# Performance work log

Measured on AMD Instinct MI355X. Metric: run time of the kernel, lower is better.

## Reference

```python
import jax, jax.numpy as jnp
import numpy as np
import math

D_MODEL = 1024
N_HEADS = 16
B, L, K = 2, 512, 4


def sinusoidal_pe(n, dim):
    # matches SinusoidalEmbedding buffer pe[:n]
    position = jnp.arange(n, dtype=jnp.float32)[:, None]
    div_term = jnp.exp(jnp.arange(0, dim, 2, dtype=jnp.float32) * (-math.log(10000.0) / dim))
    ang = position * div_term  # [n, dim//2]
    pe = jnp.zeros((n, dim), dtype=jnp.float32)
    pe = pe.at[:, 0::2].set(jnp.sin(ang))
    pe = pe.at[:, 1::2].set(jnp.cos(ang))
    return pe


def setup_inputs() -> dict:
    key = jax.random.key(0)
    ks = jax.random.split(key, 8)
    s = 1.0 / math.sqrt(D_MODEL)
    return {
        "h": jax.random.normal(ks[0], (B, L, K, D_MODEL), dtype=jnp.float32),
        "probs": jax.random.uniform(ks[1], (B, L, K), dtype=jnp.float32),
        "Wq": jax.random.normal(ks[2], (D_MODEL, D_MODEL), dtype=jnp.float32) * s,
        "bq": jnp.zeros((D_MODEL,), dtype=jnp.float32),
        "Wk": jax.random.normal(ks[3], (D_MODEL, D_MODEL), dtype=jnp.float32) * s,
        "bk": jnp.zeros((D_MODEL,), dtype=jnp.float32),
        "Wv": jax.random.normal(ks[4], (D_MODEL, D_MODEL), dtype=jnp.float32) * s,
        "bv": jnp.zeros((D_MODEL,), dtype=jnp.float32),
        "Wo": jax.random.normal(ks[5], (D_MODEL, D_MODEL), dtype=jnp.float32) * s,
        "bo": jnp.zeros((D_MODEL,), dtype=jnp.float32),
        "prob_bias_scale": jnp.float32(1.0),
        "n_heads": N_HEADS,
    }


def reference(h, probs, Wq, bq, Wk, bk, Wv, bv, Wo, bo, prob_bias_scale, n_heads):
    Bh, Lh, kh, D = h.shape
    N = Lh * kh
    hd = D // n_heads
    scale = hd ** (-0.5)

    h_flat = h.reshape(Bh, N, D) + sinusoidal_pe(N, D)[None]  # [B, N, D]
    probs_flat = probs.reshape(Bh, N)

    # torch Linear: x @ W.T + b
    q = (h_flat @ Wq.T + bq).reshape(Bh, N, n_heads, hd).transpose(0, 2, 1, 3)
    key = (h_flat @ Wk.T + bk).reshape(Bh, N, n_heads, hd).transpose(0, 2, 1, 3)
    v = (h_flat @ Wv.T + bv).reshape(Bh, N, n_heads, hd).transpose(0, 2, 1, 3)

    scores = jnp.einsum("bhnd,bhmd->bhnm", q, key) * scale  # [B,H,N,N]
    prob_bias = jnp.log(probs_flat + 1e-8)[:, None, None, :]  # bias on key axis
    scores = scores + prob_bias_scale * prob_bias
    attn = jax.nn.softmax(scores, axis=-1)  # dropout is identity in eval
    out = jnp.einsum("bhnm,bhmd->bhnd", attn, v)
    out = out.transpose(0, 2, 1, 3).reshape(Bh, N, D)
    out = out @ Wo.T + bo
    return out.reshape(Bh, Lh, kh, D)
```

## Files before the change

kernel.cpp:

```cpp
#include <hip/hip_runtime.h>

typedef _Float16 h8 __attribute__((ext_vector_type(8)));
typedef _Float16 h4 __attribute__((ext_vector_type(4)));
typedef __fp16 fp16x2 __attribute__((ext_vector_type(2)));
typedef float f32x4 __attribute__((ext_vector_type(4)));

#define NSEQ 2048
#define DMODEL 1024
#define HD 64
#define C2 0.1803368801111244f

#define OFF_HPE  (size_t)0
#define OFF_WQ   (size_t)8388608
#define OFF_WK   (size_t)10485760
#define OFF_WV   (size_t)12582912
#define OFF_WO   (size_t)14680064
#define OFF_Q    (size_t)16777216
#define OFF_K    (size_t)25165824
#define OFF_VT   (size_t)33554432
#define OFF_AO   (size_t)41943040
#define OFF_PB   (size_t)50331648

#define GLL(g, l) __builtin_amdgcn_global_load_lds( \
    (const __attribute__((address_space(1))) unsigned int*)(const void*)(g), \
    (__attribute__((address_space(3))) unsigned int*)(l), 16, 0, 0)

__global__ void hpe_kernel(const float* __restrict__ h, _Float16* __restrict__ hpe) {
    int idx = blockIdx.x * blockDim.x + threadIdx.x;
    int row = idx >> 7;
    int c8 = (idx & 127) * 8;
    int n = row & (NSEQ - 1);
    const float kL = -0.025952563241307517f;
    const float kInv2Pi = 0.15915494309189535f;
    union { float4 f4[2]; float f[8]; } in;
    in.f4[0] = *(const float4*)&h[(size_t)row * DMODEL + c8];
    in.f4[1] = *(const float4*)&h[(size_t)row * DMODEL + c8 + 4];
    union { _Float16 hh[8]; uint4 u; } out;
    #pragma unroll
    for (int p = 0; p < 4; ++p) {
        int i2 = (c8 >> 1) + p;
        float div = __builtin_amdgcn_exp2f((float)i2 * kL);
        float rev = (float)n * div * kInv2Pi;
        float rf = __builtin_amdgcn_fractf(rev);
        float s = __builtin_amdgcn_sinf(rf);
        float c = __builtin_amdgcn_cosf(rf);
        out.hh[2 * p]     = (_Float16)(in.f[2 * p] + s);
        out.hh[2 * p + 1] = (_Float16)(in.f[2 * p + 1] + c);
    }
    *(uint4*)&hpe[(size_t)row * DMODEL + c8] = out.u;
}

__global__ void cast4_kernel(const float* __restrict__ w0, const float* __restrict__ w1,
                             const float* __restrict__ w2, const float* __restrict__ w3,
                             _Float16* __restrict__ d0, _Float16* __restrict__ d1,
                             _Float16* __restrict__ d2, _Float16* __restrict__ d3) {
    int i = blockIdx.x * blockDim.x + threadIdx.x;
    int which = i >> 18, idx = i & 262143;
    const float* s = which == 0 ? w0 : which == 1 ? w1 : which == 2 ? w2 : w3;
    _Float16* d    = which == 0 ? d0 : which == 1 ? d1 : which == 2 ? d2 : d3;
    float sc = which == 0 ? C2 : 1.0f;
    float4 v = ((const float4*)s)[idx];
    union { _Float16 hh[4]; uint2 u; } o;
    o.hh[0] = (_Float16)(v.x * sc); o.hh[1] = (_Float16)(v.y * sc);
    o.hh[2] = (_Float16)(v.z * sc); o.hh[3] = (_Float16)(v.w * sc);
    ((uint2*)d)[idx] = o.u;
}

__global__ void pb_kernel(const float* __restrict__ probs, const float* __restrict__ pbs,
                          float* __restrict__ pb) {
    int i = blockIdx.x * blockDim.x + threadIdx.x;
    pb[i] = pbs[0] * log2f(probs[i] + 1e-8f);
}

__global__ __launch_bounds__(256) void gemm_qkv(
    const _Float16* __restrict__ A,
    const _Float16* __restrict__ Wqp, const _Float16* __restrict__ Wkp, const _Float16* __restrict__ Wvp,
    const float* __restrict__ bqp, const float* __restrict__ bkp, const float* __restrict__ bvp,
    _Float16* __restrict__ qb, _Float16* __restrict__ kb, _Float16* __restrict__ vt)
{
    __shared__ __align__(16) _Float16 As[128][64];
    __shared__ __align__(16) _Float16 Bs[128][64];
    int bid = blockIdx.x + 32 * blockIdx.y;
    int nf = (bid & 7) * 96 + (bid >> 3);
    int bx = nf & 31, byy = nf >> 5;
    int widx = byy >> 3;
    const _Float16* W = widx == 0 ? Wqp : widx == 1 ? Wkp : Wvp;
    const float* bias = widx == 0 ? bqp : widx == 1 ? bkp : bvp;
    float bscale = widx == 0 ? C2 : 1.0f;
    int tm = bx * 128;
    int tn = (byy & 7) * 128;
    int t = threadIdx.x;
    int wave = t >> 6, lane = t & 63;
    int wr = (wave >> 1) * 64, wc = (wave & 1) * 64;
    int lr = lane & 15, lg = lane >> 4;

    f32x4 acc[4][4] = {};

    int grow = lane >> 3;
    int gcol = (lane & 7) * 8;
    const _Float16* Aptr = A + (size_t)(tm + wave * 8 + grow) * DMODEL + gcol;
    const _Float16* Wptr = W + (size_t)(tn + wave * 8 + grow) * DMODEL + gcol;

    for (int k0 = 0; k0 < DMODEL; k0 += 64) {
        __syncthreads();
        #pragma unroll
        for (int i = 0; i < 4; ++i)
            GLL(Aptr + (size_t)i * 32 * DMODEL + k0, &As[i * 32 + wave * 8][0]);
        #pragma unroll
        for (int i = 0; i < 4; ++i)
            GLL(Wptr + (size_t)i * 32 * DMODEL + k0, &Bs[i * 32 + wave * 8][0]);
        __syncthreads();
        #pragma unroll
        for (int kk = 0; kk < 2; ++kk) {
            h8 af[4], bf[4];
            #pragma unroll
            for (int mi = 0; mi < 4; ++mi) af[mi] = *(const h8*)&As[wr + mi * 16 + lr][kk * 32 + lg * 8];
            #pragma unroll
            for (int ni = 0; ni < 4; ++ni) bf[ni] = *(const h8*)&Bs[wc + ni * 16 + lr][kk * 32 + lg * 8];
            #pragma unroll
            for (int mi = 0; mi < 4; ++mi)
                #pragma unroll
                for (int ni = 0; ni < 4; ++ni)
                    acc[mi][ni] = __builtin_amdgcn_mfma_f32_16x16x32_f16(af[mi], bf[ni], acc[mi][ni], 0, 0, 0);
        }
    }

    #pragma unroll
    for (int mi = 0; mi < 4; ++mi)
        #pragma unroll
        for (int ni = 0; ni < 4; ++ni) {
            int col = tn + wc + ni * 16 + lr;
            float bv = bias[col] * bscale;
            if (widx < 2) {
                _Float16* dst = widx == 0 ? qb : kb;
                #pragma unroll
                for (int j = 0; j < 4; ++j) {
                    int row = tm + wr + mi * 16 + lg * 4 + j;
                    dst[(size_t)row * DMODEL + col] = (_Float16)(acc[mi][ni][j] + bv);
                }
            } else {
                int row0 = tm + wr + mi * 16 + lg * 4;
                int b = row0 >> 11, n0 = row0 & 2047;
                h4 pk;
                #pragma unroll
                for (int j = 0; j < 4; ++j) pk[j] = (_Float16)(acc[mi][ni][j] + bv);
                *(h4*)&vt[((size_t)b * 1024 + col) * 2048 + n0] = pk;
            }
        }
}

__global__ __launch_bounds__(256) void gemm_ao(
    const _Float16* __restrict__ A, const _Float16* __restrict__ W,
    const float* __restrict__ bias, float* __restrict__ C)
{
    __shared__ __align__(16) _Float16 As[64][64];
    __shared__ __align__(16) _Float16 Bs[128][64];
    int bid = blockIdx.x + 64 * blockIdx.y;
    int nf = (bid & 7) * 64 + (bid >> 3);
    int tm = (nf & 63) * 64;
    int tn = (nf >> 6) * 128;
    int t = threadIdx.x;
    int wave = t >> 6, lane = t & 63;
    int wr = (wave >> 1) * 32, wc = (wave & 1) * 64;
    int lr = lane & 15, lg = lane >> 4;

    f32x4 acc[2][4] = {};

    int grow = lane >> 3;
    int gcol = (lane & 7) * 8;
    const _Float16* Aptr = A + (size_t)(tm + wave * 8 + grow) * DMODEL + gcol;
    const _Float16* Wptr = W + (size_t)(tn + wave * 8 + grow) * DMODEL + gcol;

    for (int k0 = 0; k0 < DMODEL; k0 += 64) {
        __syncthreads();
        #pragma unroll
        for (int i = 0; i < 2; ++i)
            GLL(Aptr + (size_t)i * 32 * DMODEL + k0, &As[i * 32 + wave * 8][0]);
        #pragma unroll
        for (int i = 0; i < 4; ++i)
            GLL(Wptr + (size_t)i * 32 * DMODEL + k0, &Bs[i * 32 + wave * 8][0]);
        __syncthreads();
        #pragma unroll
        for (int kk = 0; kk < 2; ++kk) {
            h8 af[2], bf[4];
            #pragma unroll
            for (int mi = 0; mi < 2; ++mi) af[mi] = *(const h8*)&As[wr + mi * 16 + lr][kk * 32 + lg * 8];
            #pragma unroll
            for (int ni = 0; ni < 4; ++ni) bf[ni] = *(const h8*)&Bs[wc + ni * 16 + lr][kk * 32 + lg * 8];
            #pragma unroll
            for (int mi = 0; mi < 2; ++mi)
                #pragma unroll
                for (int ni = 0; ni < 4; ++ni)
                    acc[mi][ni] = __builtin_amdgcn_mfma_f32_16x16x32_f16(af[mi], bf[ni], acc[mi][ni], 0, 0, 0);
        }
    }

    #pragma unroll
    for (int mi = 0; mi < 2; ++mi)
        #pragma unroll
        for (int ni = 0; ni < 4; ++ni)
            #pragma unroll
            for (int j = 0; j < 4; ++j) {
                int row = tm + wr + mi * 16 + lg * 4 + j;
                int col = tn + wc + ni * 16 + lr;
                C[(size_t)row * DMODEL + col] = acc[mi][ni][j] + bias[col];
            }
}

#define KT 64

#define SWZ(row, bytecol) ((row) * 128 + ((bytecol) ^ (((row) & 7) << 4)))

__global__ __launch_bounds__(512) void flash_kernel(
    const _Float16* __restrict__ Qb,
    const _Float16* __restrict__ Kb,
    const _Float16* __restrict__ Vt,
    const float* __restrict__ pb,
    _Float16* __restrict__ AO)
{
    __shared__ __align__(16) char KsB[2][8192];
    __shared__ __align__(16) char VsB[2][8192];
    __shared__ __align__(16) _Float16 Ps[8][16][72];

    int bid = blockIdx.x + 16 * blockIdx.y;
    int nf = (bid & 7) * 64 + (bid >> 3);
    int qx = nf & 15, bh = nf >> 4;
    int b = bh >> 4, h = bh & 15;
    int q0 = qx * 128;
    int t = threadIdx.x, wave = t >> 6, lane = t & 63;
    int lr = lane & 15, lg = lane >> 4;

    const _Float16* Khead  = Kb + (size_t)b * NSEQ * DMODEL + h * HD;
    const _Float16* Vthead = Vt + ((size_t)b * 1024 + h * HD) * NSEQ;
    const float* pbb = pb + b * NSEQ;

    const _Float16* Qrow = Qb + ((size_t)b * NSEQ + q0 + wave * 16 + lr) * DMODEL + h * HD;
    h8 qf0 = *(const h8*)&Qrow[lg * 8];
    h8 qf1 = *(const h8*)&Qrow[32 + lg * 8];

    const h8 vones = { (_Float16)1, (_Float16)1, (_Float16)1, (_Float16)1,
                       (_Float16)1, (_Float16)1, (_Float16)1, (_Float16)1 };

    float mrun = -INFINITY;
    f32x4 oacc[4] = {};
    f32x4 lsum = {};

    int srow = t >> 3;
    int schunk = (t & 7) ^ (srow & 7);
    const _Float16* Ksrc = Khead + (size_t)srow * DMODEL + schunk * 8;
    const _Float16* Vsrc = Vthead + (size_t)srow * NSEQ + schunk * 8;

    GLL(Ksrc, KsB[0] + wave * 1024);
    GLL(Vsrc, VsB[0] + wave * 1024);
    asm volatile("s_waitcnt vmcnt(0)" ::: "memory");
    __syncthreads();

    int cur = 0;
    for (int kt = 0; kt < 32; ++kt) {
        int k0 = kt * KT;
        if (kt < 31) {
            GLL(Ksrc + (size_t)(k0 + KT) * DMODEL, KsB[cur ^ 1] + wave * 1024);
            GLL(Vsrc + (k0 + KT), VsB[cur ^ 1] + wave * 1024);
        }
        const char* Kc = KsB[cur];
        const char* Vc = VsB[cur];

        f32x4 s[4];
        #pragma unroll
        for (int ci = 0; ci < 4; ++ci)
            s[ci] = *(const f32x4*)&pbb[k0 + ci * 16 + lg * 4];
        #pragma unroll
        for (int ci = 0; ci < 4; ++ci) {
            h8 kf = *(const h8*)(Kc + SWZ(ci * 16 + lr, lg * 16));
            s[ci] = __builtin_amdgcn_mfma_f32_16x16x32_f16(kf, qf0, s[ci], 0, 0, 0);
        }
        #pragma unroll
        for (int ci = 0; ci < 4; ++ci) {
            h8 kf = *(const h8*)(Kc + SWZ(ci * 16 + lr, 64 + lg * 16));
            s[ci] = __builtin_amdgcn_mfma_f32_16x16x32_f16(kf, qf1, s[ci], 0, 0, 0);
        }

        float sm = s[0][0];
        #pragma unroll
        for (int ci = 0; ci < 4; ++ci)
            #pragma unroll
            for (int j = 0; j < 4; ++j) sm = fmaxf(sm, s[ci][j]);
        sm = fmaxf(sm, __shfl_xor(sm, 16));
        sm = fmaxf(sm, __shfl_xor(sm, 32));

        bool need = __any(sm > mrun);
        float newm = need ? fmaxf(mrun, sm) : mrun;

        #pragma unroll
        for (int ci = 0; ci < 4; ++ci) {
            fp16x2 a = __builtin_amdgcn_cvt_pkrtz(__builtin_amdgcn_exp2f(s[ci][0] - newm),
                                                  __builtin_amdgcn_exp2f(s[ci][1] - newm));
            fp16x2 b2 = __builtin_amdgcn_cvt_pkrtz(__builtin_amdgcn_exp2f(s[ci][2] - newm),
                                                   __builtin_amdgcn_exp2f(s[ci][3] - newm));
            union { fp16x2 hh[2]; uint2 u; } pk;
            pk.hh[0] = a; pk.hh[1] = b2;
            *(uint2*)&Ps[wave][lr][ci * 16 + lg * 4] = pk.u;
        }

        h8 vf[2][4];
        #pragma unroll
        for (int kb = 0; kb < 2; ++kb)
            #pragma unroll
            for (int ni = 0; ni < 4; ++ni)
                vf[kb][ni] = *(const h8*)(Vc + SWZ(ni * 16 + lr, kb * 64 + lg * 16));

        if (need) {
            float fs = __builtin_amdgcn_exp2f(mrun - newm);
            mrun = newm;
            #pragma unroll
            for (int j = 0; j < 4; ++j) {
                float fsj = __shfl(fs, (lane & 48) | (lg * 4 + j), 64);
                #pragma unroll
                for (int ni = 0; ni < 4; ++ni) oacc[ni][j] *= fsj;
                lsum[j] *= fsj;
            }
        }

        asm volatile("s_waitcnt lgkmcnt(0)" ::: "memory");
        __builtin_amdgcn_sched_barrier(0);

        #pragma unroll
        for (int kb = 0; kb < 2; ++kb) {
            h8 pa = *(const h8*)&Ps[wave][lr][kb * 32 + lg * 8];
            #pragma unroll
            for (int ni = 0; ni < 4; ++ni)
                oacc[ni] = __builtin_amdgcn_mfma_f32_16x16x32_f16(pa, vf[kb][ni], oacc[ni], 0, 0, 0);
            lsum = __builtin_amdgcn_mfma_f32_16x16x32_f16(pa, vones, lsum, 0, 0, 0);
        }

        asm volatile("s_waitcnt vmcnt(0)" ::: "memory");
        __syncthreads();
        cur ^= 1;
    }

    #pragma unroll
    for (int j = 0; j < 4; ++j) {
        float inv = 1.0f / lsum[j];
        int row = q0 + wave * 16 + lg * 4 + j;
        #pragma unroll
        for (int ni = 0; ni < 4; ++ni)
            AO[((size_t)b * NSEQ + row) * DMODEL + h * HD + ni * 16 + lr] = (_Float16)(oacc[ni][j] * inv);
    }
}

extern "C" void kernel_launch(void* const* d_in, const int* in_sizes, int n_in,
                              void* d_out, int out_size, void* d_ws, size_t ws_size,
                              hipStream_t stream) {
    const float* h    = (const float*)d_in[0];
    const float* prob = (const float*)d_in[1];
    const float* Wq   = (const float*)d_in[2];
    const float* bq   = (const float*)d_in[3];
    const float* Wk   = (const float*)d_in[4];
    const float* bk   = (const float*)d_in[5];
    const float* Wv   = (const float*)d_in[6];
    const float* bv   = (const float*)d_in[7];
    const float* Wo   = (const float*)d_in[8];
    const float* bo   = (const float*)d_in[9];
    const float* pbs  = (const float*)d_in[10];

    char* ws = (char*)d_ws;
    _Float16* hpe  = (_Float16*)(ws + OFF_HPE);
    _Float16* wq16 = (_Float16*)(ws + OFF_WQ);
    _Float16* wk16 = (_Float16*)(ws + OFF_WK);
    _Float16* wv16 = (_Float16*)(ws + OFF_WV);
    _Float16* wo16 = (_Float16*)(ws + OFF_WO);
    _Float16* qb   = (_Float16*)(ws + OFF_Q);
    _Float16* kb16 = (_Float16*)(ws + OFF_K);
    _Float16* vt   = (_Float16*)(ws + OFF_VT);
    _Float16* ao   = (_Float16*)(ws + OFF_AO);
    float*    pbuf = (float*)(ws + OFF_PB);

    hpe_kernel<<<dim3(2048), dim3(256), 0, stream>>>(h, hpe);
    cast4_kernel<<<dim3(4096), dim3(256), 0, stream>>>(Wq, Wk, Wv, Wo, wq16, wk16, wv16, wo16);
    pb_kernel<<<dim3(16), dim3(256), 0, stream>>>(prob, pbs, pbuf);

    gemm_qkv<<<dim3(32, 24), dim3(256), 0, stream>>>(hpe, wq16, wk16, wv16, bq, bk, bv, qb, kb16, vt);

    flash_kernel<<<dim3(16, 32), dim3(512), 0, stream>>>(qb, kb16, vt, pbuf, ao);

    gemm_ao<<<dim3(64, 8), dim3(256), 0, stream>>>(ao, wo16, bo, (float*)d_out);
}
```

Measured before the change: 233.8 us.

## Fuse prep kernels, enlarge QKV GEMM tile, reorder flash loop sync with setprio

```diff
diff --git a/kernel.cpp b/kernel.cpp
--- a/kernel.cpp
+++ b/kernel.cpp
@@ -25,69 +25,69 @@
     (const __attribute__((address_space(1))) unsigned int*)(const void*)(g), \
     (__attribute__((address_space(3))) unsigned int*)(l), 16, 0, 0)
 
-__global__ void hpe_kernel(const float* __restrict__ h, _Float16* __restrict__ hpe) {
+__global__ void prep_kernel(const float* __restrict__ h, _Float16* __restrict__ hpe,
+                            const float* __restrict__ w0, const float* __restrict__ w1,
+                            const float* __restrict__ w2, const float* __restrict__ w3,
+                            _Float16* __restrict__ d0, _Float16* __restrict__ d1,
+                            _Float16* __restrict__ d2, _Float16* __restrict__ d3,
+                            const float* __restrict__ probs, const float* __restrict__ pbs,
+                            float* __restrict__ pb) {
     int idx = blockIdx.x * blockDim.x + threadIdx.x;
-    int row = idx >> 7;
-    int c8 = (idx & 127) * 8;
-    int n = row & (NSEQ - 1);
-    const float kL = -0.025952563241307517f;
-    const float kInv2Pi = 0.15915494309189535f;
-    union { float4 f4[2]; float f[8]; } in;
-    in.f4[0] = *(const float4*)&h[(size_t)row * DMODEL + c8];
-    in.f4[1] = *(const float4*)&h[(size_t)row * DMODEL + c8 + 4];
-    union { _Float16 hh[8]; uint4 u; } out;
-    #pragma unroll
-    for (int p = 0; p < 4; ++p) {
-        int i2 = (c8 >> 1) + p;
-        float div = __builtin_amdgcn_exp2f((float)i2 * kL);
-        float rev = (float)n * div * kInv2Pi;
-        float rf = __builtin_amdgcn_fractf(rev);
-        float s = __builtin_amdgcn_sinf(rf);
-        float c = __builtin_amdgcn_cosf(rf);
-        out.hh[2 * p]     = (_Float16)(in.f[2 * p] + s);
-        out.hh[2 * p + 1] = (_Float16)(in.f[2 * p + 1] + c);
-    }
-    *(uint4*)&hpe[(size_t)row * DMODEL + c8] = out.u;
-}
-
-__global__ void cast4_kernel(const float* __restrict__ w0, const float* __restrict__ w1,
-                             const float* __restrict__ w2, const float* __restrict__ w3,
-                             _Float16* __restrict__ d0, _Float16* __restrict__ d1,
-                             _Float16* __restrict__ d2, _Float16* __restrict__ d3) {
-    int i = blockIdx.x * blockDim.x + threadIdx.x;
-    int which = i >> 18, idx = i & 262143;
-    const float* s = which == 0 ? w0 : which == 1 ? w1 : which == 2 ? w2 : w3;
-    _Float16* d    = which == 0 ? d0 : which == 1 ? d1 : which == 2 ? d2 : d3;
-    float sc = which == 0 ? C2 : 1.0f;
-    float4 v = ((const float4*)s)[idx];
-    union { _Float16 hh[4]; uint2 u; } o;
-    o.hh[0] = (_Float16)(v.x * sc); o.hh[1] = (_Float16)(v.y * sc);
-    o.hh[2] = (_Float16)(v.z * sc); o.hh[3] = (_Float16)(v.w * sc);
-    ((uint2*)d)[idx] = o.u;
-}
-
-__global__ void pb_kernel(const float* __restrict__ probs, const float* __restrict__ pbs,
-                          float* __restrict__ pb) {
-    int i = blockIdx.x * blockDim.x + threadIdx.x;
-    pb[i] = pbs[0] * log2f(probs[i] + 1e-8f);
-}
-
-__global__ __launch_bounds__(256) void gemm_qkv(
+    if (idx < 524288) {
+        int row = idx >> 7;
+        int c8 = (idx & 127) * 8;
+        int n = row & (NSEQ - 1);
+        const float kL = -0.025952563241307517f;
+        const float kInv2Pi = 0.15915494309189535f;
+        union { float4 f4[2]; float f[8]; } in;
+        in.f4[0] = *(const float4*)&h[(size_t)row * DMODEL + c8];
+        in.f4[1] = *(const float4*)&h[(size_t)row * DMODEL + c8 + 4];
+        union { _Float16 hh[8]; uint4 u; } out;
+        #pragma unroll
+        for (int p = 0; p < 4; ++p) {
+            int i2 = (c8 >> 1) + p;
+            float div = __builtin_amdgcn_exp2f((float)i2 * kL);
+            float rev = (float)n * div * kInv2Pi;
+            float rf = __builtin_amdgcn_fractf(rev);
+            float s = __builtin_amdgcn_sinf(rf);
+            float c = __builtin_amdgcn_cosf(rf);
+            out.hh[2 * p]     = (_Float16)(in.f[2 * p] + s);
+            out.hh[2 * p + 1] = (_Float16)(in.f[2 * p + 1] + c);
+        }
+        *(uint4*)&hpe[(size_t)row * DMODEL + c8] = out.u;
+    } else if (idx < 1572864) {
+        int j = idx - 524288;
+        int which = j >> 18, i2 = j & 262143;
+        const float* s = which == 0 ? w0 : which == 1 ? w1 : which == 2 ? w2 : w3;
+        _Float16* d    = which == 0 ? d0 : which == 1 ? d1 : which == 2 ? d2 : d3;
+        float sc = which == 0 ? C2 : 1.0f;
+        float4 v = ((const float4*)s)[i2];
+        union { _Float16 hh[4]; uint2 u; } o;
+        o.hh[0] = (_Float16)(v.x * sc); o.hh[1] = (_Float16)(v.y * sc);
+        o.hh[2] = (_Float16)(v.z * sc); o.hh[3] = (_Float16)(v.w * sc);
+        ((uint2*)d)[i2] = o.u;
+    } else if (idx < 1576960) {
+        int k = idx - 1572864;
+        pb[k] = pbs[0] * log2f(probs[k] + 1e-8f);
+    }
+}
+
+__global__ __launch_bounds__(512) void gemm_qkv(
     const _Float16* __restrict__ A,
     const _Float16* __restrict__ Wqp, const _Float16* __restrict__ Wkp, const _Float16* __restrict__ Wvp,
     const float* __restrict__ bqp, const float* __restrict__ bkp, const float* __restrict__ bvp,
     _Float16* __restrict__ qb, _Float16* __restrict__ kb, _Float16* __restrict__ vt)
 {
-    __shared__ __align__(16) _Float16 As[128][64];
+    __shared__ __align__(16) _Float16 As[256][64];
     __shared__ __align__(16) _Float16 Bs[128][64];
-    int bid = blockIdx.x + 32 * blockIdx.y;
-    int nf = (bid & 7) * 96 + (bid >> 3);
-    int bx = nf & 31, byy = nf >> 5;
+    int bid = blockIdx.x;
+    int nf = (bid & 7) * 48 + (bid >> 3);
+    int bx = nf & 15, byy = nf >> 4;
     int widx = byy >> 3;
     const _Float16* W = widx == 0 ? Wqp : widx == 1 ? Wkp : Wvp;
     const float* bias = widx == 0 ? bqp : widx == 1 ? bkp : bvp;
     float bscale = widx == 0 ? C2 : 1.0f;
-    int tm = bx * 128;
+    int tm = bx * 256;
     int tn = (byy & 7) * 128;
     int t = threadIdx.x;
     int wave = t >> 6, lane = t & 63;
@@ -105,10 +105,10 @@
         __syncthreads();
         #pragma unroll
         for (int i = 0; i < 4; ++i)
-            GLL(Aptr + (size_t)i * 32 * DMODEL + k0, &As[i * 32 + wave * 8][0]);
-        #pragma unroll
-        for (int i = 0; i < 4; ++i)
-            GLL(Wptr + (size_t)i * 32 * DMODEL + k0, &Bs[i * 32 + wave * 8][0]);
+            GLL(Aptr + (size_t)i * 64 * DMODEL + k0, &As[i * 64 + wave * 8][0]);
+        #pragma unroll
+        for (int i = 0; i < 2; ++i)
+            GLL(Wptr + (size_t)i * 64 * DMODEL + k0, &Bs[i * 64 + wave * 8][0]);
         __syncthreads();
         #pragma unroll
         for (int kk = 0; kk < 2; ++kk) {
@@ -269,6 +269,7 @@
         #pragma unroll
         for (int ci = 0; ci < 4; ++ci)
             s[ci] = *(const f32x4*)&pbb[k0 + ci * 16 + lg * 4];
+        __builtin_amdgcn_s_setprio(1);
         #pragma unroll
         for (int ci = 0; ci < 4; ++ci) {
             h8 kf = *(const h8*)(Kc + SWZ(ci * 16 + lr, lg * 16));
@@ -279,6 +280,18 @@
             h8 kf = *(const h8*)(Kc + SWZ(ci * 16 + lr, 64 + lg * 16));
             s[ci] = __builtin_amdgcn_mfma_f32_16x16x32_f16(kf, qf1, s[ci], 0, 0, 0);
         }
+        __builtin_amdgcn_s_setprio(0);
+
+        h8 vf[2][4];
+        #pragma unroll
+        for (int kb = 0; kb < 2; ++kb)
+            #pragma unroll
+            for (int ni = 0; ni < 4; ++ni)
+                vf[kb][ni] = *(const h8*)(Vc + SWZ(ni * 16 + lr, kb * 64 + lg * 16));
+
+        asm volatile("s_waitcnt vmcnt(0) lgkmcnt(0)" ::: "memory");
+        __syncthreads();
+        cur ^= 1;
 
         float sm = s[0][0];
         #pragma unroll
@@ -302,13 +315,6 @@
             *(uint2*)&Ps[wave][lr][ci * 16 + lg * 4] = pk.u;
         }
 
-        h8 vf[2][4];
-        #pragma unroll
-        for (int kb = 0; kb < 2; ++kb)
-            #pragma unroll
-            for (int ni = 0; ni < 4; ++ni)
-                vf[kb][ni] = *(const h8*)(Vc + SWZ(ni * 16 + lr, kb * 64 + lg * 16));
-
         if (need) {
             float fs = __builtin_amdgcn_exp2f(mrun - newm);
             mrun = newm;
@@ -324,6 +330,7 @@
         asm volatile("s_waitcnt lgkmcnt(0)" ::: "memory");
         __builtin_amdgcn_sched_barrier(0);
 
+        __builtin_amdgcn_s_setprio(1);
         #pragma unroll
         for (int kb = 0; kb < 2; ++kb) {
             h8 pa = *(const h8*)&Ps[wave][lr][kb * 32 + lg * 8];
@@ -332,10 +339,7 @@
                 oacc[ni] = __builtin_amdgcn_mfma_f32_16x16x32_f16(pa, vf[kb][ni], oacc[ni], 0, 0, 0);
             lsum = __builtin_amdgcn_mfma_f32_16x16x32_f16(pa, vones, lsum, 0, 0, 0);
         }
-
-        asm volatile("s_waitcnt vmcnt(0)" ::: "memory");
-        __syncthreads();
-        cur ^= 1;
+        __builtin_amdgcn_s_setprio(0);
     }
 
     #pragma unroll
@@ -375,11 +379,10 @@
     _Float16* ao   = (_Float16*)(ws + OFF_AO);
     float*    pbuf = (float*)(ws + OFF_PB);
 
-    hpe_kernel<<<dim3(2048), dim3(256), 0, stream>>>(h, hpe);
-    cast4_kernel<<<dim3(4096), dim3(256), 0, stream>>>(Wq, Wk, Wv, Wo, wq16, wk16, wv16, wo16);
-    pb_kernel<<<dim3(16), dim3(256), 0, stream>>>(prob, pbs, pbuf);
-
-    gemm_qkv<<<dim3(32, 24), dim3(256), 0, stream>>>(hpe, wq16, wk16, wv16, bq, bk, bv, qb, kb16, vt);
+    prep_kernel<<<dim3(6160), dim3(256), 0, stream>>>(
+        h, hpe, Wq, Wk, Wv, Wo, wq16, wk16, wv16, wo16, prob, pbs, pbuf);
+
+    gemm_qkv<<<dim3(384), dim3(512), 0, stream>>>(hpe, wq16, wk16, wv16, bq, bk, bv, qb, kb16, vt);
 
     flash_kernel<<<dim3(16, 32), dim3(512), 0, stream>>>(qb, kb16, vt, pbuf, ao);
 
```

Measured after the change: 218.8 us. -6.4%, faster.
